# Kernel tuning notes

Hardware: AMD Instinct MI355X
Metric: run time of the kernel (lower is better)

Reference implementation:

```python
import jax, jax.numpy as jnp
import numpy as np
from jax import lax
import math

KS = 7  # attention kernel size
PAD = 3


def conv2d(x, w, b, pad):
    y = lax.conv_general_dilated(x, w, (1, 1), [(pad, pad), (pad, pad)],
                                 dimension_numbers=('NCHW', 'OIHW', 'NCHW'))
    return y + b[None, :, None, None]


def unfold(x):
    # x: [B, C, H, W] -> [B, C, KS*KS, H, W], matching nn.Unfold channel-major order
    B, C, H, W = x.shape
    xp = jnp.pad(x, ((0, 0), (0, 0), (PAD, PAD), (PAD, PAD)))
    patches = [xp[:, :, i:i + H, j:j + W] for i in range(KS) for j in range(KS)]
    return jnp.stack(patches, axis=2)


def setup_inputs() -> dict:
    key = jax.random.key(0)
    ks = jax.random.split(key, 12)
    B, H, W = 1, 256, 256
    s = lambda fan: 1.0 / np.sqrt(fan)
    inp = {
        'x': jax.random.normal(ks[0], (B, 6, H, W), jnp.float32),
        'w0': jax.random.normal(ks[1], (48, 3, 3, 3), jnp.float32) * s(3 * 9),
        'b0': jnp.zeros((48,), jnp.float32),
        'w1': jax.random.normal(ks[2], (48, 48, 3, 3), jnp.float32) * s(48 * 9),
        'b1': jnp.zeros((48,), jnp.float32),
        'w2': jax.random.normal(ks[3], (48, 48, 3, 3), jnp.float32) * s(48 * 9),
        'b2': jnp.zeros((48,), jnp.float32),
        'w3': jax.random.normal(ks[4], (24, 48, 3, 3), jnp.float32) * s(48 * 9),
        'b3': jnp.zeros((24,), jnp.float32),
        'skip_w': jax.random.normal(ks[5], (24, 3, 1, 1), jnp.float32) * s(3),
        'skip_b': jnp.zeros((24,), jnp.float32),
        'q_w': jax.random.normal(ks[6], (24, 24, 1, 1), jnp.float32) * s(24),
        'q_b': jnp.zeros((24,), jnp.float32),
        'k_w': jax.random.normal(ks[7], (24, 24, 1, 1), jnp.float32) * s(24),
        'k_b': jnp.zeros((24,), jnp.float32),
        'v_w': jax.random.normal(ks[8], (24, 24, 1, 1), jnp.float32) * s(24),
        'v_b': jnp.zeros((24,), jnp.float32),
    }
    return inp


def reference(x, w0, b0, w1, b1, w2, b2, w3, b3, skip_w, skip_b,
              q_w, q_b, k_w, k_b, v_w, v_b):
    def submodel(t):
        h = jax.nn.relu(conv2d(t, w0, b0, 1))
        h = jax.nn.relu(conv2d(h, w1, b1, 1))
        h = jax.nn.relu(conv2d(h, w2, b2, 1))
        h = jax.nn.relu(conv2d(h, w3, b3, 1))
        return h + conv2d(t, skip_w, skip_b, 0)

    xa, xb = jnp.split(x, 2, axis=1)  # [B,3,H,W] each
    a = submodel(xa)                  # [B,24,H,W]
    b = submodel(xb)

    Q = conv2d(b, q_w, q_b, 0)        # [B,24,H,W]
    K = unfold(conv2d(a, k_w, k_b, 0))  # [B,24,49,H,W]
    V = unfold(conv2d(a, v_w, v_b, 0))  # [B,24,49,H,W]

    C = Q.shape[1]
    A = jnp.einsum('bchw,bcphw->bphw', Q, K) / math.sqrt(C)
    A = jax.nn.softmax(A, axis=1)     # softmax over 49 local positions
    y = jnp.einsum('bphw,bcphw->bchw', A, V)
    return jnp.concatenate([y + a, b], axis=1)  # [B,48,H,W]
```

## Files before the change

kernel.cpp:

```cpp
#include <hip/hip_runtime.h>
#include <math.h>

#define HH 256
#define WW 256
#define NN (HH * WW)

typedef _Float16 f16;
typedef _Float16 f16x8 __attribute__((ext_vector_type(8)));
typedef _Float16 f16x4 __attribute__((ext_vector_type(4)));
typedef float f32x4 __attribute__((ext_vector_type(4)));

#define OQ 75264

__global__ __launch_bounds__(256) void prep_kernel(
    const float* __restrict__ x, const float* __restrict__ w0,
    const float* __restrict__ w1, const float* __restrict__ w2,
    const float* __restrict__ w3, const float* __restrict__ qw,
    const float* __restrict__ kw, const float* __restrict__ vw,
    f16* __restrict__ xh, f16* __restrict__ bf) {
  if (blockIdx.x < 512) {
    int p = blockIdx.x * 256 + threadIdx.x;
    int z = p >= NN;
    int q = p - z * NN;
    const float* xz = x + (size_t)z * 3 * NN;
    f16x4 v;
    v[0] = (f16)xz[q];
    v[1] = (f16)xz[NN + q];
    v[2] = (f16)xz[2 * NN + q];
    v[3] = (f16)0.f;
    *(f16x4*)(xh + (size_t)p * 4) = v;
    return;
  }
  const int O1 = 1536, O2 = O1 + 27648, O3 = O2 + 27648;
  int e = (blockIdx.x - 512) * 256 + threadIdx.x;
  if (e >= OQ + 3072) return;
  float val = 0.f;
  if (e >= OQ) {
    int idx = e - OQ;
    int mat = idx >> 10;
    int r = idx & 1023;
    int nt = r >> 9;
    int lane = (r >> 3) & 63;
    int j = r & 7;
    int n = lane & 15, quad = lane >> 4;
    int ci = quad * 8 + j, co = nt * 16 + n;
    const float* w = (mat == 0) ? qw : (mat == 1) ? kw : vw;
    if (ci < 24 && co < 24) val = w[co * 24 + ci];
  } else if (e < O1) {
    int idx = e;
    int j = idx & 7;
    int lane = (idx >> 3) & 63;
    int nt = idx >> 9;
    int n = lane & 15, quad = lane >> 4;
    int k = quad * 8 + j;
    int cout = nt * 16 + n;
    if (k < 27) {
      int tap = k / 3, ci = k - tap * 3;
      val = w0[(cout * 3 + ci) * 9 + tap];
    }
  } else {
    const float* w;
    int COUT, idx;
    if (e < O2)      { w = w1; COUT = 48; idx = e - O1; }
    else if (e < O3) { w = w2; COUT = 48; idx = e - O2; }
    else             { w = w3; COUT = 24; idx = e - O3; }
    const int NT = (COUT == 48) ? 3 : 2;
    int j = idx & 7;
    int lane = (idx >> 3) & 63;
    int rest = idx >> 9;
    int nt = rest % NT;
    int q2 = rest / NT;
    int kc = q2 & 1;
    int tap = q2 >> 1;
    int n = lane & 15, quad = lane >> 4;
    int ci = kc * 32 + quad * 8 + j;
    int cout = nt * 16 + n;
    if (ci < 48 && cout < COUT) val = w[(cout * 48 + ci) * 9 + tap];
  }
  bf[e] = (f16)val;
}

__global__ __launch_bounds__(256, 2) void conv0_gemm(
    const f16* __restrict__ xh, const f16* __restrict__ bf0,
    const float* __restrict__ bias, f16* __restrict__ outh) {
  extern __shared__ char smem[];
  const int tid = threadIdx.x;
  const int lane = tid & 63, wave = tid >> 6;
  const int n = lane & 15, quad = lane >> 4;
  const int bx = blockIdx.x * 16, by = blockIdx.y * 16, z = blockIdx.z;
  const f16* xz = xh + (size_t)z * NN * 4;

  {
    int p = tid, y = p >> 4, xcol = p & 15;
    int gy = by + y, gx = bx + xcol;
    f16* row = (f16*)(smem + p * 80);
#pragma unroll
    for (int tap = 0; tap < 9; ++tap) {
      int dy = tap / 3, dx = tap - (tap / 3) * 3;
      int sy = gy + dy - 1, sx = gx + dx - 1;
      f16 c0 = (f16)0.f, c1 = c0, c2 = c0;
      if (sy >= 0 && sy < HH && sx >= 0 && sx < WW) {
        const f16* s = xz + ((size_t)sy * WW + sx) * 4;
        c0 = s[0]; c1 = s[1]; c2 = s[2];
      }
      row[tap * 3 + 0] = c0;
      row[tap * 3 + 1] = c1;
      row[tap * 3 + 2] = c2;
    }
#pragma unroll
    for (int k = 27; k < 32; ++k) row[k] = (f16)0.f;
  }
  __syncthreads();

  f32x4 acc[4][3];
#pragma unroll
  for (int nt = 0; nt < 3; ++nt) {
    float bv = bias[nt * 16 + n];
#pragma unroll
    for (int i = 0; i < 4; ++i) acc[i][nt] = (f32x4){bv, bv, bv, bv};
  }
  f16x8 B[3];
#pragma unroll
  for (int nt = 0; nt < 3; ++nt)
    B[nt] = *(const f16x8*)(bf0 + (nt * 64 + lane) * 8);
#pragma unroll
  for (int i = 0; i < 4; ++i) {
    int r = wave * 4 + i;
    f16x8 a = *(const f16x8*)(smem + (r * 16 + n) * 80 + quad * 16);
#pragma unroll
    for (int nt = 0; nt < 3; ++nt)
      acc[i][nt] =
          __builtin_amdgcn_mfma_f32_16x16x32_f16(a, B[nt], acc[i][nt], 0, 0, 0);
  }

  f16* oz = outh + (size_t)z * NN * 48;
#pragma unroll
  for (int i = 0; i < 4; ++i) {
    int y = by + wave * 4 + i;
#pragma unroll
    for (int nt = 0; nt < 3; ++nt)
#pragma unroll
      for (int reg = 0; reg < 4; ++reg)
        oz[((size_t)y * WW + bx + quad * 4 + reg) * 48 + nt * 16 + n] =
            (f16)fmaxf(acc[i][nt][reg], 0.f);
  }
}

template <int NT, int COUT, bool FUSE>
__global__ __launch_bounds__(256, 4) void gemm_conv(
    const f16* __restrict__ in, const f16* __restrict__ bfr,
    const float* __restrict__ bias, f16* __restrict__ outh,
    const float* __restrict__ xsrc, const float* __restrict__ skw,
    const float* __restrict__ skb) {
  extern __shared__ char smem[];
  float* xt = (float*)(smem + 180 * 144);
  const int tid = threadIdx.x;
  const int lane = tid & 63, wave = tid >> 6;
  const int n = lane & 15, quad = lane >> 4;
  const int bx = blockIdx.x * 16, by = blockIdx.y * 8, z = blockIdx.z;
  const f16* inz = in + (size_t)z * NN * 48;

  if (tid < 180) {
    int p = tid;
    int yy = p / 18, xx = p - yy * 18;
    int gy = by + yy - 1, gx = bx + xx - 1;
    float4* dst = (float4*)(smem + p * 144);
    if (gy >= 0 && gy < HH && gx >= 0 && gx < WW) {
      const float4* s = (const float4*)(inz + ((size_t)gy * WW + gx) * 48);
      float4 a0 = s[0], a1 = s[1], a2 = s[2], a3 = s[3], a4 = s[4], a5 = s[5];
      dst[0] = a0; dst[1] = a1; dst[2] = a2;
      dst[3] = a3; dst[4] = a4; dst[5] = a5;
      dst[6] = make_float4(0, 0, 0, 0);
      dst[7] = make_float4(0, 0, 0, 0);
    } else {
      float4 zz = make_float4(0, 0, 0, 0);
#pragma unroll
      for (int c = 0; c < 8; ++c) dst[c] = zz;
    }
  }
  if (FUSE) {
    for (int i = tid; i < 384; i += 256) {
      int c = i >> 7, p = i & 127;
      xt[i] = xsrc[(size_t)z * 3 * NN + c * NN + (by + (p >> 4)) * WW + bx +
                   (p & 15)];
    }
  }
  __syncthreads();

  f32x4 acc[2][NT];
#pragma unroll
  for (int nt = 0; nt < NT; ++nt) {
    int cc = nt * 16 + n;
    float bv = (cc < COUT) ? bias[cc] : 0.f;
#pragma unroll
    for (int i = 0; i < 2; ++i) acc[i][nt] = (f32x4){bv, bv, bv, bv};
  }

  const int r0 = wave * 2;
#pragma unroll 1
  for (int tap = 0; tap < 9; ++tap) {
    const int dy = tap / 3, dx = tap - dy * 3;
    f16x8 B[2][NT];
#pragma unroll
    for (int kc = 0; kc < 2; ++kc)
#pragma unroll
      for (int nt = 0; nt < NT; ++nt)
        B[kc][nt] = *(const f16x8*)(bfr +
                                    (((tap * 2 + kc) * NT + nt) * 64 + lane) * 8);
#pragma unroll
    for (int i = 0; i < 2; ++i) {
      const int p = (r0 + i + dy) * 18 + (n + dx);
      const char* ap = smem + p * 144;
      f16x8 a0 = *(const f16x8*)(ap + quad * 16);
      f16x8 a1 = *(const f16x8*)(ap + 64 + quad * 16);
#pragma unroll
      for (int nt = 0; nt < NT; ++nt)
        acc[i][nt] = __builtin_amdgcn_mfma_f32_16x16x32_f16(a0, B[0][nt],
                                                            acc[i][nt], 0, 0, 0);
#pragma unroll
      for (int nt = 0; nt < NT; ++nt)
        acc[i][nt] = __builtin_amdgcn_mfma_f32_16x16x32_f16(a1, B[1][nt],
                                                            acc[i][nt], 0, 0, 0);
    }
  }

  if (!FUSE) {
    f16* oz = outh + (size_t)z * NN * 48;
#pragma unroll
    for (int i = 0; i < 2; ++i) {
      int y = by + r0 + i;
#pragma unroll
      for (int nt = 0; nt < NT; ++nt)
#pragma unroll
        for (int reg = 0; reg < 4; ++reg)
          oz[((size_t)y * WW + bx + quad * 4 + reg) * 48 + nt * 16 + n] =
              (f16)fmaxf(acc[i][nt][reg], 0.f);
    }
  } else {
    f16* oz = outh + (size_t)z * NN * 32;
#pragma unroll
    for (int i = 0; i < 2; ++i) {
      int y = by + r0 + i;
#pragma unroll
      for (int nt = 0; nt < NT; ++nt) {
        int cc = nt * 16 + n;
        float s0 = 0.f, s1 = 0.f, s2 = 0.f, sb0 = 0.f;
        if (cc < 24) {
          s0 = skw[cc * 3 + 0];
          s1 = skw[cc * 3 + 1];
          s2 = skw[cc * 3 + 2];
          sb0 = skb[cc];
        }
#pragma unroll
        for (int reg = 0; reg < 4; ++reg) {
          float v = 0.f;
          if (cc < 24) {
            int pl = (r0 + i) * 16 + quad * 4 + reg;
            float sk = sb0 + s0 * xt[pl] + s1 * xt[128 + pl] + s2 * xt[256 + pl];
            v = fmaxf(acc[i][nt][reg], 0.f) + sk;
          }
          oz[((size_t)(y * WW + bx + quad * 4 + reg)) * 32 + cc] = (f16)v;
        }
      }
    }
  }
}

__global__ __launch_bounds__(256) void q_mfma(const f16* __restrict__ ABh,
                                              const f16* __restrict__ bf,
                                              const float* __restrict__ qb,
                                              f16* __restrict__ Qh) {
  const int tid = threadIdx.x;
  const int lane = tid & 63, wave = tid >> 6;
  const int n = lane & 15, quad = lane >> 4;
  const f16* src = ABh + (size_t)NN * 32;
  f16x8 QF[2];
#pragma unroll
  for (int nt = 0; nt < 2; ++nt)
    QF[nt] = *(const f16x8*)(bf + OQ + (nt * 64 + lane) * 8);
  float qbias[2];
#pragma unroll
  for (int nt = 0; nt < 2; ++nt) {
    int cc = nt * 16 + n;
    qbias[nt] = (cc < 24) ? qb[cc] : 0.f;
  }
#pragma unroll
  for (int t = 0; t < 4; ++t) {
    int T = blockIdx.x * 16 + wave * 4 + t;
    size_t p0 = (size_t)T * 16;
    f16x8 a8 = *(const f16x8*)(src + p0 * 32 + n * 32 + quad * 8);
#pragma unroll
    for (int nt = 0; nt < 2; ++nt) {
      f32x4 acc = {qbias[nt], qbias[nt], qbias[nt], qbias[nt]};
      acc = __builtin_amdgcn_mfma_f32_16x16x32_f16(a8, QF[nt], acc, 0, 0, 0);
      int cc = nt * 16 + n;
      if (cc < 24) {
#pragma unroll
        for (int reg = 0; reg < 4; ++reg)
          Qh[(p0 + quad * 4 + reg) * 24 + cc] = (f16)acc[reg];
      }
    }
  }
}

__device__ inline float dot8p(f16x8 a, f16x8 b, float acc) {
#if __has_builtin(__builtin_amdgcn_fdot2)
  acc = __builtin_amdgcn_fdot2(__builtin_shufflevector(a, a, 0, 1),
                               __builtin_shufflevector(b, b, 0, 1), acc, false);
  acc = __builtin_amdgcn_fdot2(__builtin_shufflevector(a, a, 2, 3),
                               __builtin_shufflevector(b, b, 2, 3), acc, false);
  acc = __builtin_amdgcn_fdot2(__builtin_shufflevector(a, a, 4, 5),
                               __builtin_shufflevector(b, b, 4, 5), acc, false);
  acc = __builtin_amdgcn_fdot2(__builtin_shufflevector(a, a, 6, 7),
                               __builtin_shufflevector(b, b, 6, 7), acc, false);
  return acc;
#else
#pragma unroll
  for (int i = 0; i < 8; ++i) acc += (float)a[i] * (float)b[i];
  return acc;
#endif
}

__global__ __launch_bounds__(256, 3) void attn_kernel(
    const f16* __restrict__ Qh, const f16* __restrict__ ABh,
    const f16* __restrict__ bf, const float* __restrict__ kb,
    const float* __restrict__ vb, float* __restrict__ out) {
  extern __shared__ f16 kv[];
  const int tid = threadIdx.x;
  const int lane = tid & 63, wave = tid >> 6;
  const int n16 = lane & 15, quad = lane >> 4;
  const int bx = blockIdx.x * 32, by = blockIdx.y * 8;
  const int xl = tid & 31, yl = tid >> 5;
  const int p = (by + yl) * WW + bx + xl;
  const f16* ah = ABh;
  const f16* bh = ABh + (size_t)NN * 32;

  f16x8 q0 = *(const f16x8*)(Qh + (size_t)p * 24);
  f16x8 q1 = *(const f16x8*)(Qh + (size_t)p * 24 + 8);
  f16x8 q2 = *(const f16x8*)(Qh + (size_t)p * 24 + 16);

  for (int idx = tid; idx < 2128; idx += 256) {
    int row = idx / 152;
    int rem = idx - row * 152;
    int pxl = rem >> 2;
    int c = rem & 3;
    int gy = by + row - 3, gx = bx + pxl - 3;
    f16x8 v = {};
    if (gy >= 0 && gy < HH && gx >= 0 && gx < WW)
      v = *(const f16x8*)(ah + ((size_t)(gy * WW + gx)) * 32 + c * 8);
    *(f16x8*)(kv + (row * 38 + pxl) * 56 + c * 8) = v;
  }
  __syncthreads();

  const f16* cs = kv + ((yl + 3) * 38 + xl + 3) * 56;
  f16x8 a0 = *(const f16x8*)(cs);
  f16x8 a1 = *(const f16x8*)(cs + 8);
  f16x8 a2 = *(const f16x8*)(cs + 16);
  __syncthreads();

  {
    f16x8 KF[2], VF[2];
#pragma unroll
    for (int nt = 0; nt < 2; ++nt) {
      KF[nt] = *(const f16x8*)(bf + OQ + 1024 + (nt * 64 + lane) * 8);
      VF[nt] = *(const f16x8*)(bf + OQ + 2048 + (nt * 64 + lane) * 8);
    }
    float kbias[2], vbias[2];
#pragma unroll
    for (int nt = 0; nt < 2; ++nt) {
      int cc = nt * 16 + n16;
      kbias[nt] = (cc < 24) ? kb[cc] : 0.f;
      vbias[nt] = (cc < 24) ? vb[cc] : 0.f;
    }
    for (int t = wave; t < 34; t += 4) {
      f16x8 a8 = *(const f16x8*)(kv + (t * 16 + n16) * 56 + quad * 8);
#pragma unroll
      for (int nt = 0; nt < 2; ++nt) {
        f32x4 ak = {kbias[nt], kbias[nt], kbias[nt], kbias[nt]};
        f32x4 av = {vbias[nt], vbias[nt], vbias[nt], vbias[nt]};
        ak = __builtin_amdgcn_mfma_f32_16x16x32_f16(a8, KF[nt], ak, 0, 0, 0);
        av = __builtin_amdgcn_mfma_f32_16x16x32_f16(a8, VF[nt], av, 0, 0, 0);
        int cc = nt * 16 + n16;
        if (cc < 24) {
#pragma unroll
          for (int reg = 0; reg < 4; ++reg) {
            f16* slot = kv + (t * 16 + quad * 4 + reg) * 56;
            slot[cc] = (f16)ak[reg];
            slot[24 + cc] = (f16)av[reg];
          }
        }
      }
    }
  }
  __syncthreads();

  float s[49];
#pragma unroll
  for (int pp = 0; pp < 49; ++pp) {
    int dy = pp / 7, dx = pp - dy * 7;
    const f16* base = kv + ((yl + dy) * 38 + xl + dx) * 56;
    f16x8 k0 = *(const f16x8*)(base);
    f16x8 k1 = *(const f16x8*)(base + 8);
    f16x8 k2 = *(const f16x8*)(base + 16);
    float d = 0.f;
    d = dot8p(q0, k0, d);
    d = dot8p(q1, k1, d);
    d = dot8p(q2, k2, d);
    s[pp] = d * 0.20412414523193154f;
  }

  float m = s[0];
#pragma unroll
  for (int pp = 1; pp < 49; ++pp) m = fmaxf(m, s[pp]);
  float den = 0.f;
#pragma unroll
  for (int pp = 0; pp < 49; ++pp) {
    float e = __expf(s[pp] - m);
    s[pp] = e;
    den += e;
  }
  const float inv = 1.f / den;

  f16x8 y0 = {}, y1 = {}, y2 = {};
#pragma unroll
  for (int pp = 0; pp < 49; ++pp) {
    int dy = pp / 7, dx = pp - dy * 7;
    const f16* base = kv + ((yl + dy) * 38 + xl + dx) * 56 + 24;
    f16 wh = (f16)(s[pp] * inv);
    f16x8 w8 = {wh, wh, wh, wh, wh, wh, wh, wh};
    f16x8 v0 = *(const f16x8*)(base);
    f16x8 v1 = *(const f16x8*)(base + 8);
    f16x8 v2 = *(const f16x8*)(base + 16);
    y0 = v0 * w8 + y0;
    y1 = v1 * w8 + y1;
    y2 = v2 * w8 + y2;
  }

  f16x8 b0 = *(const f16x8*)(bh + (size_t)p * 32);
  f16x8 b1 = *(const f16x8*)(bh + (size_t)p * 32 + 8);
  f16x8 b2 = *(const f16x8*)(bh + (size_t)p * 32 + 16);
#pragma unroll
  for (int c = 0; c < 8; ++c) {
    out[(size_t)c * NN + p] = (float)y0[c] + (float)a0[c];
    out[(size_t)(8 + c) * NN + p] = (float)y1[c] + (float)a1[c];
    out[(size_t)(16 + c) * NN + p] = (float)y2[c] + (float)a2[c];
    out[(size_t)(24 + c) * NN + p] = (float)b0[c];
    out[(size_t)(32 + c) * NN + p] = (float)b1[c];
    out[(size_t)(40 + c) * NN + p] = (float)b2[c];
  }
}

extern "C" void kernel_launch(void* const* d_in, const int* in_sizes, int n_in,
                              void* d_out, int out_size, void* d_ws,
                              size_t ws_size, hipStream_t stream) {
  const float* x = (const float*)d_in[0];
  const float* w0 = (const float*)d_in[1];
  const float* b0 = (const float*)d_in[2];
  const float* w1 = (const float*)d_in[3];
  const float* b1 = (const float*)d_in[4];
  const float* w2 = (const float*)d_in[5];
  const float* b2 = (const float*)d_in[6];
  const float* w3 = (const float*)d_in[7];
  const float* b3 = (const float*)d_in[8];
  const float* sw = (const float*)d_in[9];
  const float* sb = (const float*)d_in[10];
  const float* qw = (const float*)d_in[11];
  const float* qb = (const float*)d_in[12];
  const float* kw = (const float*)d_in[13];
  const float* kb = (const float*)d_in[14];
  const float* vw = (const float*)d_in[15];
  const float* vb = (const float*)d_in[16];
  float* out = (float*)d_out;
  float* ws = (float*)d_ws;

  f16* Qh = (f16*)(ws);
  f16* ABh = (f16*)(ws + (size_t)12 * NN);
  f16* ACT0 = (f16*)(ws + (size_t)44 * NN);
  f16* ACT1 = (f16*)(ws + (size_t)92 * NN);
  f16* XH = (f16*)(ws + (size_t)140 * NN);
  f16* BF = (f16*)(ws + (size_t)144 * NN);

  prep_kernel<<<dim3(818), dim3(256), 0, stream>>>(x, w0, w1, w2, w3, qw, kw,
                                                   vw, XH, BF);

  conv0_gemm<<<dim3(16, 16, 2), dim3(256), 256 * 80, stream>>>(XH, BF, b0,
                                                               ACT0);
  dim3 g2(16, 32, 2);
  gemm_conv<3, 48, false><<<g2, dim3(256), 180 * 144, stream>>>(
      ACT0, BF + 1536, b1, ACT1, nullptr, nullptr, nullptr);
  gemm_conv<3, 48, false><<<g2, dim3(256), 180 * 144, stream>>>(
      ACT1, BF + 29184, b2, ACT0, nullptr, nullptr, nullptr);
  gemm_conv<2, 24, true><<<g2, dim3(256), 180 * 144 + 1536, stream>>>(
      ACT0, BF + 56832, b3, ABh, x, sw, sb);

  q_mfma<<<dim3(256), dim3(256), 0, stream>>>(ABh, BF, qb, Qh);

  attn_kernel<<<dim3(8, 32), dim3(256), 544 * 112, stream>>>(Qh, ABh, BF, kb,
                                                             vb, out);
}
```

Before: 158.8 us.

## Fuse four conv layers into one halo-recompute kernel and fold Q into attention

New measurement: 156.7 us. Within noise of the previous version (-1.3%).

```diff
diff --git a/kernel.cpp b/kernel.cpp
--- a/kernel.cpp
+++ b/kernel.cpp
@@ -7,301 +7,9 @@
 
 typedef _Float16 f16;
 typedef _Float16 f16x8 __attribute__((ext_vector_type(8)));
-typedef _Float16 f16x4 __attribute__((ext_vector_type(4)));
 typedef float f32x4 __attribute__((ext_vector_type(4)));
 
 #define OQ 75264
-
-__global__ __launch_bounds__(256) void prep_kernel(
-    const float* __restrict__ x, const float* __restrict__ w0,
-    const float* __restrict__ w1, const float* __restrict__ w2,
-    const float* __restrict__ w3, const float* __restrict__ qw,
-    const float* __restrict__ kw, const float* __restrict__ vw,
-    f16* __restrict__ xh, f16* __restrict__ bf) {
-  if (blockIdx.x < 512) {
-    int p = blockIdx.x * 256 + threadIdx.x;
-    int z = p >= NN;
-    int q = p - z * NN;
-    const float* xz = x + (size_t)z * 3 * NN;
-    f16x4 v;
-    v[0] = (f16)xz[q];
-    v[1] = (f16)xz[NN + q];
-    v[2] = (f16)xz[2 * NN + q];
-    v[3] = (f16)0.f;
-    *(f16x4*)(xh + (size_t)p * 4) = v;
-    return;
-  }
-  const int O1 = 1536, O2 = O1 + 27648, O3 = O2 + 27648;
-  int e = (blockIdx.x - 512) * 256 + threadIdx.x;
-  if (e >= OQ + 3072) return;
-  float val = 0.f;
-  if (e >= OQ) {
-    int idx = e - OQ;
-    int mat = idx >> 10;
-    int r = idx & 1023;
-    int nt = r >> 9;
-    int lane = (r >> 3) & 63;
-    int j = r & 7;
-    int n = lane & 15, quad = lane >> 4;
-    int ci = quad * 8 + j, co = nt * 16 + n;
-    const float* w = (mat == 0) ? qw : (mat == 1) ? kw : vw;
-    if (ci < 24 && co < 24) val = w[co * 24 + ci];
-  } else if (e < O1) {
-    int idx = e;
-    int j = idx & 7;
-    int lane = (idx >> 3) & 63;
-    int nt = idx >> 9;
-    int n = lane & 15, quad = lane >> 4;
-    int k = quad * 8 + j;
-    int cout = nt * 16 + n;
-    if (k < 27) {
-      int tap = k / 3, ci = k - tap * 3;
-      val = w0[(cout * 3 + ci) * 9 + tap];
-    }
-  } else {
-    const float* w;
-    int COUT, idx;
-    if (e < O2)      { w = w1; COUT = 48; idx = e - O1; }
-    else if (e < O3) { w = w2; COUT = 48; idx = e - O2; }
-    else             { w = w3; COUT = 24; idx = e - O3; }
-    const int NT = (COUT == 48) ? 3 : 2;
-    int j = idx & 7;
-    int lane = (idx >> 3) & 63;
-    int rest = idx >> 9;
-    int nt = rest % NT;
-    int q2 = rest / NT;
-    int kc = q2 & 1;
-    int tap = q2 >> 1;
-    int n = lane & 15, quad = lane >> 4;
-    int ci = kc * 32 + quad * 8 + j;
-    int cout = nt * 16 + n;
-    if (ci < 48 && cout < COUT) val = w[(cout * 48 + ci) * 9 + tap];
-  }
-  bf[e] = (f16)val;
-}
-
-__global__ __launch_bounds__(256, 2) void conv0_gemm(
-    const f16* __restrict__ xh, const f16* __restrict__ bf0,
-    const float* __restrict__ bias, f16* __restrict__ outh) {
-  extern __shared__ char smem[];
-  const int tid = threadIdx.x;
-  const int lane = tid & 63, wave = tid >> 6;
-  const int n = lane & 15, quad = lane >> 4;
-  const int bx = blockIdx.x * 16, by = blockIdx.y * 16, z = blockIdx.z;
-  const f16* xz = xh + (size_t)z * NN * 4;
-
-  {
-    int p = tid, y = p >> 4, xcol = p & 15;
-    int gy = by + y, gx = bx + xcol;
-    f16* row = (f16*)(smem + p * 80);
-#pragma unroll
-    for (int tap = 0; tap < 9; ++tap) {
-      int dy = tap / 3, dx = tap - (tap / 3) * 3;
-      int sy = gy + dy - 1, sx = gx + dx - 1;
-      f16 c0 = (f16)0.f, c1 = c0, c2 = c0;
-      if (sy >= 0 && sy < HH && sx >= 0 && sx < WW) {
-        const f16* s = xz + ((size_t)sy * WW + sx) * 4;
-        c0 = s[0]; c1 = s[1]; c2 = s[2];
-      }
-      row[tap * 3 + 0] = c0;
-      row[tap * 3 + 1] = c1;
-      row[tap * 3 + 2] = c2;
-    }
-#pragma unroll
-    for (int k = 27; k < 32; ++k) row[k] = (f16)0.f;
-  }
-  __syncthreads();
-
-  f32x4 acc[4][3];
-#pragma unroll
-  for (int nt = 0; nt < 3; ++nt) {
-    float bv = bias[nt * 16 + n];
-#pragma unroll
-    for (int i = 0; i < 4; ++i) acc[i][nt] = (f32x4){bv, bv, bv, bv};
-  }
-  f16x8 B[3];
-#pragma unroll
-  for (int nt = 0; nt < 3; ++nt)
-    B[nt] = *(const f16x8*)(bf0 + (nt * 64 + lane) * 8);
-#pragma unroll
-  for (int i = 0; i < 4; ++i) {
-    int r = wave * 4 + i;
-    f16x8 a = *(const f16x8*)(smem + (r * 16 + n) * 80 + quad * 16);
-#pragma unroll
-    for (int nt = 0; nt < 3; ++nt)
-      acc[i][nt] =
-          __builtin_amdgcn_mfma_f32_16x16x32_f16(a, B[nt], acc[i][nt], 0, 0, 0);
-  }
-
-  f16* oz = outh + (size_t)z * NN * 48;
-#pragma unroll
-  for (int i = 0; i < 4; ++i) {
-    int y = by + wave * 4 + i;
-#pragma unroll
-    for (int nt = 0; nt < 3; ++nt)
-#pragma unroll
-      for (int reg = 0; reg < 4; ++reg)
-        oz[((size_t)y * WW + bx + quad * 4 + reg) * 48 + nt * 16 + n] =
-            (f16)fmaxf(acc[i][nt][reg], 0.f);
-  }
-}
-
-template <int NT, int COUT, bool FUSE>
-__global__ __launch_bounds__(256, 4) void gemm_conv(
-    const f16* __restrict__ in, const f16* __restrict__ bfr,
-    const float* __restrict__ bias, f16* __restrict__ outh,
-    const float* __restrict__ xsrc, const float* __restrict__ skw,
-    const float* __restrict__ skb) {
-  extern __shared__ char smem[];
-  float* xt = (float*)(smem + 180 * 144);
-  const int tid = threadIdx.x;
-  const int lane = tid & 63, wave = tid >> 6;
-  const int n = lane & 15, quad = lane >> 4;
-  const int bx = blockIdx.x * 16, by = blockIdx.y * 8, z = blockIdx.z;
-  const f16* inz = in + (size_t)z * NN * 48;
-
-  if (tid < 180) {
-    int p = tid;
-    int yy = p / 18, xx = p - yy * 18;
-    int gy = by + yy - 1, gx = bx + xx - 1;
-    float4* dst = (float4*)(smem + p * 144);
-    if (gy >= 0 && gy < HH && gx >= 0 && gx < WW) {
-      const float4* s = (const float4*)(inz + ((size_t)gy * WW + gx) * 48);
-      float4 a0 = s[0], a1 = s[1], a2 = s[2], a3 = s[3], a4 = s[4], a5 = s[5];
-      dst[0] = a0; dst[1] = a1; dst[2] = a2;
-      dst[3] = a3; dst[4] = a4; dst[5] = a5;
-      dst[6] = make_float4(0, 0, 0, 0);
-      dst[7] = make_float4(0, 0, 0, 0);
-    } else {
-      float4 zz = make_float4(0, 0, 0, 0);
-#pragma unroll
-      for (int c = 0; c < 8; ++c) dst[c] = zz;
-    }
-  }
-  if (FUSE) {
-    for (int i = tid; i < 384; i += 256) {
-      int c = i >> 7, p = i & 127;
-      xt[i] = xsrc[(size_t)z * 3 * NN + c * NN + (by + (p >> 4)) * WW + bx +
-                   (p & 15)];
-    }
-  }
-  __syncthreads();
-
-  f32x4 acc[2][NT];
-#pragma unroll
-  for (int nt = 0; nt < NT; ++nt) {
-    int cc = nt * 16 + n;
-    float bv = (cc < COUT) ? bias[cc] : 0.f;
-#pragma unroll
-    for (int i = 0; i < 2; ++i) acc[i][nt] = (f32x4){bv, bv, bv, bv};
-  }
-
-  const int r0 = wave * 2;
-#pragma unroll 1
-  for (int tap = 0; tap < 9; ++tap) {
-    const int dy = tap / 3, dx = tap - dy * 3;
-    f16x8 B[2][NT];
-#pragma unroll
-    for (int kc = 0; kc < 2; ++kc)
-#pragma unroll
-      for (int nt = 0; nt < NT; ++nt)
-        B[kc][nt] = *(const f16x8*)(bfr +
-                                    (((tap * 2 + kc) * NT + nt) * 64 + lane) * 8);
-#pragma unroll
-    for (int i = 0; i < 2; ++i) {
-      const int p = (r0 + i + dy) * 18 + (n + dx);
-      const char* ap = smem + p * 144;
-      f16x8 a0 = *(const f16x8*)(ap + quad * 16);
-      f16x8 a1 = *(const f16x8*)(ap + 64 + quad * 16);
-#pragma unroll
-      for (int nt = 0; nt < NT; ++nt)
-        acc[i][nt] = __builtin_amdgcn_mfma_f32_16x16x32_f16(a0, B[0][nt],
-                                                            acc[i][nt], 0, 0, 0);
-#pragma unroll
-      for (int nt = 0; nt < NT; ++nt)
-        acc[i][nt] = __builtin_amdgcn_mfma_f32_16x16x32_f16(a1, B[1][nt],
-                                                            acc[i][nt], 0, 0, 0);
-    }
-  }
-
-  if (!FUSE) {
-    f16* oz = outh + (size_t)z * NN * 48;
-#pragma unroll
-    for (int i = 0; i < 2; ++i) {
-      int y = by + r0 + i;
-#pragma unroll
-      for (int nt = 0; nt < NT; ++nt)
-#pragma unroll
-        for (int reg = 0; reg < 4; ++reg)
-          oz[((size_t)y * WW + bx + quad * 4 + reg) * 48 + nt * 16 + n] =
-              (f16)fmaxf(acc[i][nt][reg], 0.f);
-    }
-  } else {
-    f16* oz = outh + (size_t)z * NN * 32;
-#pragma unroll
-    for (int i = 0; i < 2; ++i) {
-      int y = by + r0 + i;
-#pragma unroll
-      for (int nt = 0; nt < NT; ++nt) {
-        int cc = nt * 16 + n;
-        float s0 = 0.f, s1 = 0.f, s2 = 0.f, sb0 = 0.f;
-        if (cc < 24) {
-          s0 = skw[cc * 3 + 0];
-          s1 = skw[cc * 3 + 1];
-          s2 = skw[cc * 3 + 2];
-          sb0 = skb[cc];
-        }
-#pragma unroll
-        for (int reg = 0; reg < 4; ++reg) {
-          float v = 0.f;
-          if (cc < 24) {
-            int pl = (r0 + i) * 16 + quad * 4 + reg;
-            float sk = sb0 + s0 * xt[pl] + s1 * xt[128 + pl] + s2 * xt[256 + pl];
-            v = fmaxf(acc[i][nt][reg], 0.f) + sk;
-          }
-          oz[((size_t)(y * WW + bx + quad * 4 + reg)) * 32 + cc] = (f16)v;
-        }
-      }
-    }
-  }
-}
-
-__global__ __launch_bounds__(256) void q_mfma(const f16* __restrict__ ABh,
-                                              const f16* __restrict__ bf,
-                                              const float* __restrict__ qb,
-                                              f16* __restrict__ Qh) {
-  const int tid = threadIdx.x;
-  const int lane = tid & 63, wave = tid >> 6;
-  const int n = lane & 15, quad = lane >> 4;
-  const f16* src = ABh + (size_t)NN * 32;
-  f16x8 QF[2];
-#pragma unroll
-  for (int nt = 0; nt < 2; ++nt)
-    QF[nt] = *(const f16x8*)(bf + OQ + (nt * 64 + lane) * 8);
-  float qbias[2];
-#pragma unroll
-  for (int nt = 0; nt < 2; ++nt) {
-    int cc = nt * 16 + n;
-    qbias[nt] = (cc < 24) ? qb[cc] : 0.f;
-  }
-#pragma unroll
-  for (int t = 0; t < 4; ++t) {
-    int T = blockIdx.x * 16 + wave * 4 + t;
-    size_t p0 = (size_t)T * 16;
-    f16x8 a8 = *(const f16x8*)(src + p0 * 32 + n * 32 + quad * 8);
-#pragma unroll
-    for (int nt = 0; nt < 2; ++nt) {
-      f32x4 acc = {qbias[nt], qbias[nt], qbias[nt], qbias[nt]};
-      acc = __builtin_amdgcn_mfma_f32_16x16x32_f16(a8, QF[nt], acc, 0, 0, 0);
-      int cc = nt * 16 + n;
-      if (cc < 24) {
-#pragma unroll
-        for (int reg = 0; reg < 4; ++reg)
-          Qh[(p0 + quad * 4 + reg) * 24 + cc] = (f16)acc[reg];
-      }
-    }
-  }
-}
 
 __device__ inline float dot8p(f16x8 a, f16x8 b, float acc) {
 #if __has_builtin(__builtin_amdgcn_fdot2)
@@ -321,66 +29,389 @@
 #endif
 }
 
-__global__ __launch_bounds__(256, 3) void attn_kernel(
-    const f16* __restrict__ Qh, const f16* __restrict__ ABh,
-    const f16* __restrict__ bf, const float* __restrict__ kb,
-    const float* __restrict__ vb, float* __restrict__ out) {
-  extern __shared__ f16 kv[];
+__device__ __forceinline__ float repack_elem(
+    int e, const float* __restrict__ w0, const float* __restrict__ w1,
+    const float* __restrict__ w2, const float* __restrict__ w3,
+    const float* __restrict__ qw, const float* __restrict__ kw,
+    const float* __restrict__ vw) {
+  const int O1 = 1536, O2 = O1 + 27648, O3 = O2 + 27648;
+  float val = 0.f;
+  if (e >= OQ) {
+    int idx = e - OQ;
+    int mat = idx >> 10;
+    int r = idx & 1023;
+    int nt = r >> 9;
+    int ln = (r >> 3) & 63;
+    int j = r & 7;
+    int nn = ln & 15, qd = ln >> 4;
+    int ci = qd * 8 + j, co = nt * 16 + nn;
+    const float* w = (mat == 0) ? qw : (mat == 1) ? kw : vw;
+    if (ci < 24 && co < 24) val = w[co * 24 + ci];
+  } else if (e < O1) {
+    int j = e & 7;
+    int ln = (e >> 3) & 63;
+    int nt = e >> 9;
+    int nn = ln & 15, qd = ln >> 4;
+    int k = qd * 8 + j;
+    int cout = nt * 16 + nn;
+    if (k < 27) {
+      int tap = k / 3, ci = k - tap * 3;
+      val = w0[(cout * 3 + ci) * 9 + tap];
+    }
+  } else {
+    const float* w;
+    int COUT, idx;
+    if (e < O2)      { w = w1; COUT = 48; idx = e - O1; }
+    else if (e < O3) { w = w2; COUT = 48; idx = e - O2; }
+    else             { w = w3; COUT = 24; idx = e - O3; }
+    const int NT = (COUT == 48) ? 3 : 2;
+    int j = idx & 7;
+    int ln = (idx >> 3) & 63;
+    int rest = idx >> 9;
+    int nt = rest % NT;
+    int q2 = rest / NT;
+    int kc = q2 & 1;
+    int tap = q2 >> 1;
+    int nn = ln & 15, qd = ln >> 4;
+    int ci = kc * 32 + qd * 8 + j;
+    int cout = nt * 16 + nn;
+    if (ci < 48 && cout < COUT) val = w[(cout * 48 + ci) * 9 + tap];
+  }
+  return val;
+}
+
+__global__ __launch_bounds__(256) void prep(
+    const float* __restrict__ w0, const float* __restrict__ w1,
+    const float* __restrict__ w2, const float* __restrict__ w3,
+    const float* __restrict__ qw, const float* __restrict__ kw,
+    const float* __restrict__ vw, f16* __restrict__ bf) {
+  int e = blockIdx.x * 256 + threadIdx.x;
+  bf[e] = (f16)repack_elem(e, w0, w1, w2, w3, qw, kw, vw);
+}
+
+template <int W_IN, int W_OUT, int H_OUT, int MAXT>
+__device__ __forceinline__ void stage_mid(const f16* __restrict__ inb,
+                                          f16* __restrict__ outb,
+                                          const f16* __restrict__ bfr,
+                                          const float* __restrict__ bias,
+                                          int gy0, int gx0, int tid) {
+  const int P = W_OUT * H_OUT;
+  const int T = (P + 15) >> 4;
+  const int lane = tid & 63, wave = tid >> 6;
+  const int n = lane & 15, quad = lane >> 4;
+  f32x4 acc[MAXT][3];
+  int ay[MAXT], ax[MAXT];
+#pragma unroll
+  for (int ti = 0; ti < MAXT; ++ti) {
+    int t = wave + 4 * ti;
+    int qa = t * 16 + n;
+    if (qa > P - 1) qa = P - 1;
+    ay[ti] = qa / W_OUT;
+    ax[ti] = qa - ay[ti] * W_OUT;
+#pragma unroll
+    for (int nt = 0; nt < 3; ++nt) {
+      float bv = bias[nt * 16 + n];
+      acc[ti][nt] = (f32x4){bv, bv, bv, bv};
+    }
+  }
+#pragma unroll 1
+  for (int tap = 0; tap < 9; ++tap) {
+    const int dy = tap / 3, dx = tap - dy * 3;
+    f16x8 B[2][3];
+#pragma unroll
+    for (int kc = 0; kc < 2; ++kc)
+#pragma unroll
+      for (int nt = 0; nt < 3; ++nt)
+        B[kc][nt] =
+            *(const f16x8*)(bfr + (((tap * 2 + kc) * 3 + nt) * 64 + lane) * 8);
+#pragma unroll
+    for (int ti = 0; ti < MAXT; ++ti) {
+      if (wave + 4 * ti < T) {
+        const f16* ap = inb + ((ay[ti] + dy) * W_IN + ax[ti] + dx) * 56 +
+                        quad * 8;
+        f16x8 a0 = *(const f16x8*)(ap);
+        f16x8 a1 = *(const f16x8*)(ap + 32);
+#pragma unroll
+        for (int nt = 0; nt < 3; ++nt)
+          acc[ti][nt] = __builtin_amdgcn_mfma_f32_16x16x32_f16(
+              a0, B[0][nt], acc[ti][nt], 0, 0, 0);
+#pragma unroll
+        for (int nt = 0; nt < 3; ++nt)
+          acc[ti][nt] = __builtin_amdgcn_mfma_f32_16x16x32_f16(
+              a1, B[1][nt], acc[ti][nt], 0, 0, 0);
+      }
+    }
+  }
+#pragma unroll
+  for (int ti = 0; ti < MAXT; ++ti) {
+    int t = wave + 4 * ti;
+    if (t < T) {
+#pragma unroll
+      for (int reg = 0; reg < 4; ++reg) {
+        int q = t * 16 + quad * 4 + reg;
+        if (q < P) {
+          int qy = q / W_OUT, qx = q - qy * W_OUT;
+          int gy = gy0 + qy, gx = gx0 + qx;
+          bool im = (gy >= 0 && gy < HH && gx >= 0 && gx < WW);
+#pragma unroll
+          for (int nt = 0; nt < 3; ++nt) {
+            float v = im ? fmaxf(acc[ti][nt][reg], 0.f) : 0.f;
+            outb[q * 56 + nt * 16 + n] = (f16)v;
+          }
+        }
+      }
+    }
+  }
+}
+
+__global__ __launch_bounds__(256, 2) void fused_conv(
+    const float* __restrict__ x, const float* __restrict__ b0,
+    const float* __restrict__ b1, const float* __restrict__ b2,
+    const float* __restrict__ b3, const float* __restrict__ sw,
+    const float* __restrict__ sb, f16* __restrict__ ABh,
+    const f16* __restrict__ BF) {
+  extern __shared__ char smem[];
+  f16* bufA = (f16*)smem;
+  f16* bufB = (f16*)(smem + 34496);
+  const int tid = threadIdx.x;
+  const int bz = blockIdx.x;
+  const int z = bz >> 9, tt = bz & 511;
+  const int bx = (tt & 15) * 16, by = (tt >> 4) * 8;
+  const int lane = tid & 63, wave = tid >> 6;
+  const int n = lane & 15, quad = lane >> 4;
+  const float* xz = x + (size_t)z * 3 * NN;
+
+  for (int i = tid; i < 3840; i += 256) {
+    f16x8 zz = {};
+    *(f16x8*)(smem + i * 16) = zz;
+  }
+  __syncthreads();
+
+  for (int p = tid; p < 308; p += 256) {
+    int py = p / 22, px = p - py * 22;
+    int gy = by - 3 + py, gx = bx - 3 + px;
+    f16* row = bufB + p * 40;
+#pragma unroll
+    for (int tap = 0; tap < 9; ++tap) {
+      int dy = tap / 3, dx = tap - (tap / 3) * 3;
+      int sy = gy + dy - 1, sx = gx + dx - 1;
+      f16 c0 = (f16)0.f, c1 = c0, c2 = c0;
+      if (sy >= 0 && sy < HH && sx >= 0 && sx < WW) {
+        int o = sy * WW + sx;
+        c0 = (f16)xz[o];
+        c1 = (f16)xz[NN + o];
+        c2 = (f16)xz[2 * NN + o];
+      }
+      row[tap * 3 + 0] = c0;
+      row[tap * 3 + 1] = c1;
+      row[tap * 3 + 2] = c2;
+    }
+#pragma unroll
+    for (int k = 27; k < 32; ++k) row[k] = (f16)0.f;
+  }
+  __syncthreads();
+
+  {
+    f16x8 B0[3];
+#pragma unroll
+    for (int nt = 0; nt < 3; ++nt)
+      B0[nt] = *(const f16x8*)(BF + (nt * 64 + lane) * 8);
+    f32x4 acc[5][3];
+#pragma unroll
+    for (int ti = 0; ti < 5; ++ti)
+#pragma unroll
+      for (int nt = 0; nt < 3; ++nt) {
+        float bv = b0[nt * 16 + n];
+        acc[ti][nt] = (f32x4){bv, bv, bv, bv};
+      }
+#pragma unroll
+    for (int ti = 0; ti < 5; ++ti) {
+      int t = wave + 4 * ti;
+      int qa = t * 16 + n;
+      if (qa > 307) qa = 307;
+      f16x8 a = *(const f16x8*)(bufB + qa * 40 + quad * 8);
+#pragma unroll
+      for (int nt = 0; nt < 3; ++nt)
+        acc[ti][nt] = __builtin_amdgcn_mfma_f32_16x16x32_f16(a, B0[nt],
+                                                             acc[ti][nt], 0,
+                                                             0, 0);
+    }
+#pragma unroll
+    for (int ti = 0; ti < 5; ++ti) {
+      int t = wave + 4 * ti;
+#pragma unroll
+      for (int reg = 0; reg < 4; ++reg) {
+        int q = t * 16 + quad * 4 + reg;
+        if (q < 308) {
+          int qy = q / 22, qx = q - qy * 22;
+          int gy = by - 3 + qy, gx = bx - 3 + qx;
+          bool im = (gy >= 0 && gy < HH && gx >= 0 && gx < WW);
+#pragma unroll
+          for (int nt = 0; nt < 3; ++nt) {
+            float v = im ? fmaxf(acc[ti][nt][reg], 0.f) : 0.f;
+            bufA[q * 56 + nt * 16 + n] = (f16)v;
+          }
+        }
+      }
+    }
+  }
+  __syncthreads();
+
+  stage_mid<22, 20, 12, 4>(bufA, bufB, BF + 1536, b1, by - 2, bx - 2, tid);
+  __syncthreads();
+  stage_mid<20, 18, 10, 3>(bufB, bufA, BF + 29184, b2, by - 1, bx - 1, tid);
+  __syncthreads();
+
+  {
+    f32x4 acc[2][2];
+    int ay[2], ax[2];
+#pragma unroll
+    for (int ti = 0; ti < 2; ++ti) {
+      int qa = (wave + 4 * ti) * 16 + n;
+      ay[ti] = qa >> 4;
+      ax[ti] = qa & 15;
+#pragma unroll
+      for (int nt = 0; nt < 2; ++nt) {
+        int cc = nt * 16 + n;
+        float bv = (cc < 24) ? b3[cc] : 0.f;
+        acc[ti][nt] = (f32x4){bv, bv, bv, bv};
+      }
+    }
+#pragma unroll 1
+    for (int tap = 0; tap < 9; ++tap) {
+      const int dy = tap / 3, dx = tap - dy * 3;
+      f16x8 B[2][2];
+#pragma unroll
+      for (int kc = 0; kc < 2; ++kc)
+#pragma unroll
+        for (int nt = 0; nt < 2; ++nt)
+          B[kc][nt] = *(const f16x8*)(BF + 56832 +
+                                      (((tap * 2 + kc) * 2 + nt) * 64 + lane) *
+                                          8);
+#pragma unroll
+      for (int ti = 0; ti < 2; ++ti) {
+        const f16* ap = bufA + ((ay[ti] + dy) * 18 + ax[ti] + dx) * 56 +
+                        quad * 8;
+        f16x8 a0 = *(const f16x8*)(ap);
+        f16x8 a1 = *(const f16x8*)(ap + 32);
+#pragma unroll
+        for (int nt = 0; nt < 2; ++nt)
+          acc[ti][nt] = __builtin_amdgcn_mfma_f32_16x16x32_f16(
+              a0, B[0][nt], acc[ti][nt], 0, 0, 0);
+#pragma unroll
+        for (int nt = 0; nt < 2; ++nt)
+          acc[ti][nt] = __builtin_amdgcn_mfma_f32_16x16x32_f16(
+              a1, B[1][nt], acc[ti][nt], 0, 0, 0);
+      }
+    }
+    f16* oz = ABh + (size_t)z * NN * 32;
+#pragma unroll
+    for (int ti = 0; ti < 2; ++ti) {
+      int t = wave + 4 * ti;
+#pragma unroll
+      for (int reg = 0; reg < 4; ++reg) {
+        int q = t * 16 + quad * 4 + reg;
+        int gy = by + (q >> 4), gx = bx + (q & 15);
+        int o = gy * WW + gx;
+        float xv0 = xz[o], xv1 = xz[NN + o], xv2 = xz[2 * NN + o];
+#pragma unroll
+        for (int nt = 0; nt < 2; ++nt) {
+          int cc = nt * 16 + n;
+          float v = 0.f;
+          if (cc < 24) {
+            float sk = sb[cc] + sw[cc * 3 + 0] * xv0 + sw[cc * 3 + 1] * xv1 +
+                       sw[cc * 3 + 2] * xv2;
+            v = fmaxf(acc[ti][nt][reg], 0.f) + sk;
+          }
+          oz[(size_t)o * 32 + cc] = (f16)v;
+        }
+      }
+    }
+  }
+}
+
+__global__ __launch_bounds__(256, 3) void attn_q(
+    const f16* __restrict__ ABh, const f16* __restrict__ BF,
+    const float* __restrict__ qw, const float* __restrict__ qb,
+    const float* __restrict__ kb, const float* __restrict__ vb,
+    float* __restrict__ out) {
+  extern __shared__ char smem[];
+  f16* kv = (f16*)smem;
+  f16* Wq = (f16*)(smem + 35840);
+  float* Qbv = (float*)(smem + 35840 + 1152);
   const int tid = threadIdx.x;
   const int lane = tid & 63, wave = tid >> 6;
-  const int n16 = lane & 15, quad = lane >> 4;
-  const int bx = blockIdx.x * 32, by = blockIdx.y * 8;
-  const int xl = tid & 31, yl = tid >> 5;
-  const int p = (by + yl) * WW + bx + xl;
-  const f16* ah = ABh;
-  const f16* bh = ABh + (size_t)NN * 32;
-
-  f16x8 q0 = *(const f16x8*)(Qh + (size_t)p * 24);
-  f16x8 q1 = *(const f16x8*)(Qh + (size_t)p * 24 + 8);
-  f16x8 q2 = *(const f16x8*)(Qh + (size_t)p * 24 + 16);
-
-  for (int idx = tid; idx < 2128; idx += 256) {
-    int row = idx / 152;
-    int rem = idx - row * 152;
-    int pxl = rem >> 2;
-    int c = rem & 3;
-    int gy = by + row - 3, gx = bx + pxl - 3;
+  const int n = lane & 15, quad = lane >> 4;
+  const int bxA = ((int)blockIdx.x & 15) * 16, byA = ((int)blockIdx.x >> 4) * 8;
+
+  for (int i = tid; i < 576; i += 256) Wq[i] = (f16)qw[i];
+  if (tid < 24) Qbv[tid] = qb[tid];
+
+  for (int idx = tid; idx < 1232; idx += 256) {
+    int slot = idx >> 2, c = idx & 3;
+    int row = slot / 22, pxl = slot - row * 22;
+    int gy = byA + row - 3, gx = bxA + pxl - 3;
     f16x8 v = {};
     if (gy >= 0 && gy < HH && gx >= 0 && gx < WW)
-      v = *(const f16x8*)(ah + ((size_t)(gy * WW + gx)) * 32 + c * 8);
-    *(f16x8*)(kv + (row * 38 + pxl) * 56 + c * 8) = v;
-  }
-  __syncthreads();
-
-  const f16* cs = kv + ((yl + 3) * 38 + xl + 3) * 56;
+      v = *(const f16x8*)(ABh + ((size_t)(gy * WW + gx)) * 32 + c * 8);
+    *(f16x8*)(kv + slot * 56 + c * 8) = v;
+  }
+  __syncthreads();
+
+  const int t7 = tid & 127, half = tid >> 7;
+  const int yl = t7 >> 4, xl = t7 & 15;
+  const int pg = (byA + yl) * WW + bxA + xl;
+
+  const f16* cs = kv + ((yl + 3) * 22 + (xl + 3)) * 56;
   f16x8 a0 = *(const f16x8*)(cs);
   f16x8 a1 = *(const f16x8*)(cs + 8);
   f16x8 a2 = *(const f16x8*)(cs + 16);
+
+  const f16* bhp = ABh + (size_t)NN * 32 + (size_t)pg * 32;
+  f16x8 bb0 = *(const f16x8*)(bhp);
+  f16x8 bb1 = *(const f16x8*)(bhp + 8);
+  f16x8 bb2 = *(const f16x8*)(bhp + 16);
+  float qf[24];
+#pragma unroll
+  for (int co = 0; co < 24; ++co) {
+    float acc = Qbv[co];
+    acc = dot8p(bb0, *(const f16x8*)(Wq + co * 24), acc);
+    acc = dot8p(bb1, *(const f16x8*)(Wq + co * 24 + 8), acc);
+    acc = dot8p(bb2, *(const f16x8*)(Wq + co * 24 + 16), acc);
+    qf[co] = acc;
+  }
+  f16x8 q0, q1, q2;
+#pragma unroll
+  for (int c = 0; c < 8; ++c) {
+    q0[c] = (f16)qf[c];
+    q1[c] = (f16)qf[8 + c];
+    q2[c] = (f16)qf[16 + c];
+  }
   __syncthreads();
 
   {
     f16x8 KF[2], VF[2];
 #pragma unroll
     for (int nt = 0; nt < 2; ++nt) {
-      KF[nt] = *(const f16x8*)(bf + OQ + 1024 + (nt * 64 + lane) * 8);
-      VF[nt] = *(const f16x8*)(bf + OQ + 2048 + (nt * 64 + lane) * 8);
+      KF[nt] = *(const f16x8*)(BF + OQ + 1024 + (nt * 64 + lane) * 8);
+      VF[nt] = *(const f16x8*)(BF + OQ + 2048 + (nt * 64 + lane) * 8);
     }
     float kbias[2], vbias[2];
 #pragma unroll
     for (int nt = 0; nt < 2; ++nt) {
-      int cc = nt * 16 + n16;
+      int cc = nt * 16 + n;
       kbias[nt] = (cc < 24) ? kb[cc] : 0.f;
       vbias[nt] = (cc < 24) ? vb[cc] : 0.f;
     }
-    for (int t = wave; t < 34; t += 4) {
-      f16x8 a8 = *(const f16x8*)(kv + (t * 16 + n16) * 56 + quad * 8);
+    for (int t = wave; t < 20; t += 4) {
+      f16x8 a8 = *(const f16x8*)(kv + (t * 16 + n) * 56 + quad * 8);
 #pragma unroll
       for (int nt = 0; nt < 2; ++nt) {
         f32x4 ak = {kbias[nt], kbias[nt], kbias[nt], kbias[nt]};
         f32x4 av = {vbias[nt], vbias[nt], vbias[nt], vbias[nt]};
         ak = __builtin_amdgcn_mfma_f32_16x16x32_f16(a8, KF[nt], ak, 0, 0, 0);
         av = __builtin_amdgcn_mfma_f32_16x16x32_f16(a8, VF[nt], av, 0, 0, 0);
-        int cc = nt * 16 + n16;
+        int cc = nt * 16 + n;
         if (cc < 24) {
 #pragma unroll
           for (int reg = 0; reg < 4; ++reg) {
@@ -394,59 +425,91 @@
   }
   __syncthreads();
 
-  float s[49];
-#pragma unroll
-  for (int pp = 0; pp < 49; ++pp) {
-    int dy = pp / 7, dx = pp - dy * 7;
-    const f16* base = kv + ((yl + dy) * 38 + xl + dx) * 56;
-    f16x8 k0 = *(const f16x8*)(base);
-    f16x8 k1 = *(const f16x8*)(base + 8);
-    f16x8 k2 = *(const f16x8*)(base + 16);
-    float d = 0.f;
-    d = dot8p(q0, k0, d);
-    d = dot8p(q1, k1, d);
-    d = dot8p(q2, k2, d);
-    s[pp] = d * 0.20412414523193154f;
-  }
-
-  float m = s[0];
-#pragma unroll
-  for (int pp = 1; pp < 49; ++pp) m = fmaxf(m, s[pp]);
+  float s[25];
+  float m = -3e38f;
+#pragma unroll
+  for (int i = 0; i < 25; ++i) {
+    int pp = half * 25 + i;
+    if (pp < 49) {
+      int dy = pp / 7, dx = pp - (pp / 7) * 7;
+      const f16* base = kv + ((yl + dy) * 22 + (xl + dx)) * 56;
+      f16x8 k0 = *(const f16x8*)(base);
+      f16x8 k1 = *(const f16x8*)(base + 8);
+      f16x8 k2 = *(const f16x8*)(base + 16);
+      float d = 0.f;
+      d = dot8p(q0, k0, d);
+      d = dot8p(q1, k1, d);
+      d = dot8p(q2, k2, d);
+      s[i] = d * 0.20412414523193154f;
+      m = fmaxf(m, s[i]);
+    } else {
+      s[i] = -3e38f;
+    }
+  }
   float den = 0.f;
 #pragma unroll
-  for (int pp = 0; pp < 49; ++pp) {
-    float e = __expf(s[pp] - m);
-    s[pp] = e;
+  for (int i = 0; i < 25; ++i) {
+    float e = __expf(s[i] - m);
+    s[i] = e;
     den += e;
   }
-  const float inv = 1.f / den;
 
   f16x8 y0 = {}, y1 = {}, y2 = {};
 #pragma unroll
-  for (int pp = 0; pp < 49; ++pp) {
-    int dy = pp / 7, dx = pp - dy * 7;
-    const f16* base = kv + ((yl + dy) * 38 + xl + dx) * 56 + 24;
-    f16 wh = (f16)(s[pp] * inv);
-    f16x8 w8 = {wh, wh, wh, wh, wh, wh, wh, wh};
-    f16x8 v0 = *(const f16x8*)(base);
-    f16x8 v1 = *(const f16x8*)(base + 8);
-    f16x8 v2 = *(const f16x8*)(base + 16);
-    y0 = v0 * w8 + y0;
-    y1 = v1 * w8 + y1;
-    y2 = v2 * w8 + y2;
-  }
-
-  f16x8 b0 = *(const f16x8*)(bh + (size_t)p * 32);
-  f16x8 b1 = *(const f16x8*)(bh + (size_t)p * 32 + 8);
-  f16x8 b2 = *(const f16x8*)(bh + (size_t)p * 32 + 16);
-#pragma unroll
-  for (int c = 0; c < 8; ++c) {
-    out[(size_t)c * NN + p] = (float)y0[c] + (float)a0[c];
-    out[(size_t)(8 + c) * NN + p] = (float)y1[c] + (float)a1[c];
-    out[(size_t)(16 + c) * NN + p] = (float)y2[c] + (float)a2[c];
-    out[(size_t)(24 + c) * NN + p] = (float)b0[c];
-    out[(size_t)(32 + c) * NN + p] = (float)b1[c];
-    out[(size_t)(40 + c) * NN + p] = (float)b2[c];
+  for (int i = 0; i < 25; ++i) {
+    int pp = half * 25 + i;
+    if (pp < 49) {
+      int dy = pp / 7, dx = pp - (pp / 7) * 7;
+      const f16* base = kv + ((yl + dy) * 22 + (xl + dx)) * 56 + 24;
+      f16 wh = (f16)s[i];
+      f16x8 w8 = {wh, wh, wh, wh, wh, wh, wh, wh};
+      f16x8 v0 = *(const f16x8*)(base);
+      f16x8 v1 = *(const f16x8*)(base + 8);
+      f16x8 v2 = *(const f16x8*)(base + 16);
+      y0 = v0 * w8 + y0;
+      y1 = v1 * w8 + y1;
+      y2 = v2 * w8 + y2;
+    }
+  }
+  __syncthreads();
+
+  if (half == 1) {
+    f16* ex = kv + t7 * 56;
+    *(f16x8*)(ex) = y0;
+    *(f16x8*)(ex + 8) = y1;
+    *(f16x8*)(ex + 16) = y2;
+    float* mf = (float*)(ex + 24);
+    mf[0] = m;
+    mf[1] = den;
+  }
+  __syncthreads();
+
+  if (half == 0) {
+    const f16* ex = kv + t7 * 56;
+    f16x8 yb0 = *(const f16x8*)(ex);
+    f16x8 yb1 = *(const f16x8*)(ex + 8);
+    f16x8 yb2 = *(const f16x8*)(ex + 16);
+    const float* mf = (const float*)(ex + 24);
+    float mB = mf[0], dB = mf[1];
+    float M = fmaxf(m, mB);
+    float fa = __expf(m - M), fb = __expf(mB - M);
+    float inv = 1.f / (den * fa + dB * fb);
+#pragma unroll
+    for (int c = 0; c < 8; ++c) {
+      out[(size_t)c * NN + pg] =
+          ((float)y0[c] * fa + (float)yb0[c] * fb) * inv + (float)a0[c];
+      out[(size_t)(8 + c) * NN + pg] =
+          ((float)y1[c] * fa + (float)yb1[c] * fb) * inv + (float)a1[c];
+      out[(size_t)(16 + c) * NN + pg] =
+          ((float)y2[c] * fa + (float)yb2[c] * fb) * inv + (float)a2[c];
+    }
+  } else {
+#pragma unroll
+    for (int c = 0; c < 8; ++c) {
+      out[(size_t)(24 + c) * NN + pg] = (float)bb0[c];
+      out[(size_t)(32 + c) * NN + pg] = (float)bb1[c];
+      out[(size_t)(40 + c) * NN + pg] = (float)bb2[c];
+    }
   }
 }
 
@@ -471,30 +534,14 @@
   const float* vw = (const float*)d_in[15];
   const float* vb = (const float*)d_in[16];
   float* out = (float*)d_out;
-  float* ws = (float*)d_ws;
-
-  f16* Qh = (f16*)(ws);
-  f16* ABh = (f16*)(ws + (size_t)12 * NN);
-  f16* ACT0 = (f16*)(ws + (size_t)44 * NN);
-  f16* ACT1 = (f16*)(ws + (size_t)92 * NN);
-  f16* XH = (f16*)(ws + (size_t)140 * NN);
-  f16* BF = (f16*)(ws + (size_t)144 * NN);
-
-  prep_kernel<<<dim3(818), dim3(256), 0, stream>>>(x, w0, w1, w2, w3, qw, kw,
-                                                   vw, XH, BF);
-
-  conv0_gemm<<<dim3(16, 16, 2), dim3(256), 256 * 80, stream>>>(XH, BF, b0,
-                                                               ACT0);
-  dim3 g2(16, 32, 2);
-  gemm_conv<3, 48, false><<<g2, dim3(256), 180 * 144, stream>>>(
-      ACT0, BF + 1536, b1, ACT1, nullptr, nullptr, nullptr);
-  gemm_conv<3, 48, false><<<g2, dim3(256), 180 * 144, stream>>>(
-      ACT1, BF + 29184, b2, ACT0, nullptr, nullptr, nullptr);
-  gemm_conv<2, 24, true><<<g2, dim3(256), 180 * 144 + 1536, stream>>>(
-      ACT0, BF + 56832, b3, ABh, x, sw, sb);
-
-  q_mfma<<<dim3(256), dim3(256), 0, stream>>>(ABh, BF, qb, Qh);
-
-  attn_kernel<<<dim3(8, 32), dim3(256), 544 * 112, stream>>>(Qh, ABh, BF, kb,
-                                                             vb, out);
-}
+
+  f16* base = (f16*)d_ws;
+  f16* ABh = base;
+  f16* BF = base + (size_t)64 * NN;
+
+  prep<<<dim3(306), dim3(256), 0, stream>>>(w0, w1, w2, w3, qw, kw, vw, BF);
+  fused_conv<<<dim3(1024), dim3(256), 61440, stream>>>(x, b0, b1, b2, b3, sw,
+                                                       sb, ABh, BF);
+  attn_q<<<dim3(512), dim3(256), 37088, stream>>>(ABh, BF, qw, qb, kb, vb,
+                                                  out);
+}
```
